# Optimization experiments

Measured on AMD Instinct MI355X. Metric: run time of the kernel, lower is better.

The kernel has to match this reference:

```python
import jax, jax.numpy as jnp
import numpy as np

N_NODES = 50000
N_EDGES = 800000
FEAT = 128
HIDDEN = 128
N_GRAPHS = 128


def setup_inputs() -> dict:
    key = jax.random.key(0)
    ks = jax.random.split(key, 12)
    x = jax.random.normal(ks[0], (N_NODES, FEAT), dtype=jnp.float32)
    # edges with no self loops (original add_remaining_self_loops drops existing
    # self loops and re-adds all of them; generating loop-free edges keeps the
    # reference simple and exactly equivalent)
    row = jax.random.randint(ks[1], (N_EDGES,), 0, N_NODES)
    off = jax.random.randint(ks[2], (N_EDGES,), 1, N_NODES)
    col = (row + off) % N_NODES
    edge_index = jnp.stack([row, col]).astype(jnp.int64)
    batch = jnp.sort(jax.random.randint(ks[3], (N_NODES,), 0, N_GRAPHS)).astype(jnp.int64)
    def glorot(k, fan_in, fan_out):
        s = np.sqrt(6.0 / (fan_in + fan_out))
        return jax.random.uniform(k, (fan_in, fan_out), jnp.float32, -s, s)
    W0 = glorot(ks[4], FEAT, HIDDEN)
    W1 = glorot(ks[5], HIDDEN, HIDDEN)
    W2 = glorot(ks[6], HIDDEN, HIDDEN)
    b0 = jnp.zeros((HIDDEN,), jnp.float32)
    b1 = jnp.zeros((HIDDEN,), jnp.float32)
    b2 = jnp.zeros((HIDDEN,), jnp.float32)
    return {"x": x, "edge_index": edge_index, "batch": batch,
            "W0": W0, "b0": b0, "W1": W1, "b1": b1, "W2": W2, "b2": b2}


def _gcn_norm(edge_index, num_nodes):
    # add self loops, compute symmetric normalization coeffs per edge
    loops = jnp.arange(num_nodes, dtype=edge_index.dtype)
    row = jnp.concatenate([edge_index[0], loops])
    col = jnp.concatenate([edge_index[1], loops])
    w = jnp.ones(row.shape[0], jnp.float32)
    deg = jax.ops.segment_sum(w, col, num_segments=num_nodes)
    dis = jnp.where(deg > 0, jax.lax.rsqrt(jnp.maximum(deg, 1e-30)), 0.0)
    norm = dis[row] * dis[col]
    return row, col, norm


def _gcn_layer(x, row, col, norm, W, b, num_nodes):
    h = x @ W                               # [N, H]
    msg = norm[:, None] * h[row]            # gather + scale  [E+N, H]
    out = jax.ops.segment_sum(msg, col, num_segments=num_nodes) + b
    return jax.nn.relu(out)


def reference(x, edge_index, batch, W0, b0, W1, b1, W2, b2):
    n = x.shape[0]
    row, col, norm = _gcn_norm(edge_index, n)
    x1 = _gcn_layer(x, row, col, norm, W0, b0, n)
    x2 = _gcn_layer(x1, row, col, norm, W1, b1, n)
    x3 = _gcn_layer(x2, row, col, norm, W2, b2, n)
    pools = [jax.ops.segment_sum(xi, batch, num_segments=N_GRAPHS)
             for xi in (x1, x2, x3)]
    global_rep = jnp.concatenate(pools, axis=1)  # [G, 3*H]
    return (global_rep, x3)
```

## Files before the change

### kernel.cpp

```cpp
#include <hip/hip_runtime.h>
#include <hip/hip_fp16.h>

#define N_NODES 50000
#define N_EDGES 800000
#define F 128
#define NG 128
#define POOL_W (3*F)
#define SCAN_CHUNK 1024
#define SCAN_BLKS ((N_NODES + SCAN_CHUNK - 1) / SCAN_CHUNK)

typedef _Float16 f16x8 __attribute__((ext_vector_type(8)));
typedef float f32x2 __attribute__((ext_vector_type(2)));
typedef float f32x4 __attribute__((ext_vector_type(4)));

__device__ __forceinline__ unsigned short f2h16(float f) {
    return __half_as_ushort(__float2half_rn(f));
}
__device__ __forceinline__ unsigned pkh2(float a, float b) {
    auto v = __builtin_amdgcn_cvt_pkrtz(a, b);
    union { decltype(v) h; unsigned u; } t;
    t.h = v;
    return t.u;
}
__device__ __forceinline__ void fma8(float* acc, uint2 v, float n) {
    f32x2 d;
    d = __builtin_amdgcn_cvt_pk_f32_fp8((int)v.x, false);
    acc[0] = fmaf(n, d[0], acc[0]); acc[1] = fmaf(n, d[1], acc[1]);
    d = __builtin_amdgcn_cvt_pk_f32_fp8((int)v.x, true);
    acc[2] = fmaf(n, d[0], acc[2]); acc[3] = fmaf(n, d[1], acc[3]);
    d = __builtin_amdgcn_cvt_pk_f32_fp8((int)v.y, false);
    acc[4] = fmaf(n, d[0], acc[4]); acc[5] = fmaf(n, d[1], acc[5]);
    d = __builtin_amdgcn_cvt_pk_f32_fp8((int)v.y, true);
    acc[6] = fmaf(n, d[0], acc[6]); acc[7] = fmaf(n, d[1], acc[7]);
}
__device__ __forceinline__ unsigned char f2fp8(float f) {
    return (unsigned char)(__builtin_amdgcn_cvt_pk_fp8_f32(f, f, 0, false) & 0xFF);
}
__device__ __forceinline__ float nrm_of(unsigned u) {
    return __half2float(__ushort_as_half((unsigned short)(u & 0xFFFFu)));
}

__global__ void k_init(int* __restrict__ cnt, float* __restrict__ pool,
                       const float* __restrict__ W0, const float* __restrict__ W1,
                       const float* __restrict__ W2, unsigned short* __restrict__ WT) {
    int i = blockIdx.x * 256 + threadIdx.x;
    if (i < N_NODES) cnt[i] = 0;
    if (i < NG * POOL_W) {
        pool[i] = 0.0f;
        int w = i >> 14, r = i & 16383;
        int k = r >> 7, c = r & 127;
        const float* W = (w == 0) ? W0 : (w == 1) ? W1 : W2;
        WT[(size_t)w * F * F + c * F + k] = f2h16(W[r]);
    }
}

__global__ void k_hist(const int* __restrict__ col, int* __restrict__ cnt,
                       unsigned short* __restrict__ seq) {
    int e2 = (blockIdx.x * 256 + threadIdx.x) * 2;
    if (e2 >= N_EDGES) return;
    int2 cc = *(const int2*)&col[e2];
    unsigned short s0 = (unsigned short)atomicAdd(&cnt[cc.x], 1);
    unsigned short s1 = (unsigned short)atomicAdd(&cnt[cc.y], 1);
    *(ushort2*)&seq[e2] = make_ushort2(s0, s1);
}

__global__ __launch_bounds__(256) void k_scan_red(const int* __restrict__ cnt,
                                                  int* __restrict__ part) {
    __shared__ int wsum[4];
    int i4 = blockIdx.x * SCAN_CHUNK + threadIdx.x * 4;
    int s;
    if (i4 + 3 < N_NODES) {
        int4 v = *(const int4*)&cnt[i4];
        s = v.x + v.y + v.z + v.w;
    } else {
        s = 0;
        #pragma unroll
        for (int j = 0; j < 4; ++j) if (i4 + j < N_NODES) s += cnt[i4 + j];
    }
    #pragma unroll
    for (int o = 32; o > 0; o >>= 1) s += __shfl_xor(s, o, 64);
    int lane = threadIdx.x & 63, w = threadIdx.x >> 6;
    if (lane == 0) wsum[w] = s;
    __syncthreads();
    if (threadIdx.x == 0) part[blockIdx.x] = wsum[0] + wsum[1] + wsum[2] + wsum[3];
}

__global__ __launch_bounds__(256) void k_scan_fin(const int* __restrict__ cnt,
                                                  const int* __restrict__ part,
                                                  int* __restrict__ rowptr,
                                                  float* __restrict__ dis) {
    __shared__ int wsum[4];
    __shared__ int sBase;
    int lane = threadIdx.x & 63, w = threadIdx.x >> 6;

    if (w == 0) {
        int v = (lane < SCAN_BLKS) ? part[lane] : 0;
        int s = v;
        #pragma unroll
        for (int o = 1; o < 64; o <<= 1) {
            int t = __shfl_up(s, o, 64);
            if (lane >= o) s += t;
        }
        if (lane == (int)blockIdx.x) sBase = s - v;
    }

    int i4 = blockIdx.x * SCAN_CHUNK + threadIdx.x * 4;
    int v[4];
    #pragma unroll
    for (int j = 0; j < 4; ++j) v[j] = (i4 + j < N_NODES) ? cnt[i4 + j] : 0;
    int ts = v[0] + v[1] + v[2] + v[3];
    int incl = ts;
    #pragma unroll
    for (int o = 1; o < 64; o <<= 1) {
        int t = __shfl_up(incl, o, 64);
        if (lane >= o) incl += t;
    }
    if (lane == 63) wsum[w] = incl;
    __syncthreads();
    if (threadIdx.x == 0) {
        int a = 0;
        #pragma unroll
        for (int t = 0; t < 4; ++t) { int b = wsum[t]; wsum[t] = a; a += b; }
    }
    __syncthreads();
    int base = sBase + wsum[w] + (incl - ts);
    int pre = 0;
    #pragma unroll
    for (int j = 0; j < 4; ++j) {
        int i = i4 + j;
        if (i <= N_NODES) rowptr[i] = base + pre;
        if (i < N_NODES) dis[i] = rsqrtf((float)v[j] + 1.0f);
        pre += v[j];
    }
}

__global__ void k_fill(const int* __restrict__ row, const int* __restrict__ col,
                       const unsigned short* __restrict__ seq,
                       const int* __restrict__ rowptr, const float* __restrict__ dis,
                       unsigned* __restrict__ csr) {
    int e2 = (blockIdx.x * 256 + threadIdx.x) * 2;
    if (e2 >= N_EDGES) return;
    int2 rr = *(const int2*)&row[e2];
    int2 cc = *(const int2*)&col[e2];
    ushort2 ss = *(const ushort2*)&seq[e2];
    int p0 = rowptr[cc.x] + (int)ss.x;
    csr[p0] = ((unsigned)rr.x << 16) | (unsigned)f2h16(dis[rr.x] * dis[cc.x]);
    int p1 = rowptr[cc.y] + (int)ss.y;
    csr[p1] = ((unsigned)rr.y << 16) | (unsigned)f2h16(dis[rr.y] * dis[cc.y]);
}

template <typename AIN>
__global__ __launch_bounds__(256) void k_gemm(const AIN* __restrict__ A,
                                              const unsigned short* __restrict__ WT,
                                              unsigned char* __restrict__ H) {
    __shared__ unsigned short sWT[F * 136];
    for (int t = threadIdx.x; t < F * 16; t += 256) {
        int c = t >> 4, ch = t & 15;
        *(uint4*)&sWT[c * 136 + ch * 8] = *(const uint4*)&WT[(size_t)c * F + ch * 8];
    }
    __syncthreads();

    int wave = threadIdx.x >> 6, lane = threadIdx.x & 63;
    int m = lane & 15, q = lane >> 4;
    int row = blockIdx.x * 64 + wave * 16 + m;
    int arow = (row < N_NODES) ? row : (N_NODES - 1);

    f32x4 acc[8];
    #pragma unroll
    for (int c = 0; c < 8; ++c) acc[c] = 0.f;

    #pragma unroll
    for (int kk = 0; kk < 4; ++kk) {
        int k0 = kk * 32 + q * 8;
        f16x8 a;
        if constexpr (sizeof(AIN) == 4) {
            const float* ap = &A[(size_t)arow * F + k0];
            float4 a0 = *(const float4*)ap;
            float4 a1 = *(const float4*)(ap + 4);
            a[0] = (_Float16)a0.x; a[1] = (_Float16)a0.y;
            a[2] = (_Float16)a0.z; a[3] = (_Float16)a0.w;
            a[4] = (_Float16)a1.x; a[5] = (_Float16)a1.y;
            a[6] = (_Float16)a1.z; a[7] = (_Float16)a1.w;
        } else {
            a = *(const f16x8*)&A[(size_t)arow * F + k0];
        }
        #pragma unroll
        for (int c = 0; c < 8; ++c) {
            f16x8 b = *(const f16x8*)&sWT[(c * 16 + m) * 136 + k0];
            acc[c] = __builtin_amdgcn_mfma_f32_16x16x32_f16(a, b, acc[c], 0, 0, 0);
        }
    }

    int rbase = blockIdx.x * 64 + wave * 16 + q * 4;
    #pragma unroll
    for (int c = 0; c < 8; ++c) {
        #pragma unroll
        for (int r = 0; r < 4; ++r) {
            int rr = rbase + r;
            if (rr < N_NODES) H[(size_t)rr * F + c * 16 + m] = f2fp8(acc[c][r]);
        }
    }
}

template <typename OUT>
__global__ __launch_bounds__(256) void k_agg(const unsigned char* __restrict__ h,
                                             const float* __restrict__ dis,
                                             const int* __restrict__ rowptr,
                                             const unsigned* __restrict__ csr,
                                             const float* __restrict__ bias,
                                             const int* __restrict__ batch,
                                             OUT* __restrict__ xout,
                                             float* __restrict__ pool) {
    int wave = threadIdx.x >> 6;
    int lane = threadIdx.x & 63;
    int g = lane >> 4;
    int l = lane & 15;
    int node = blockIdx.x * 4 + wave;

    float acc[8] = {0.f, 0.f, 0.f, 0.f, 0.f, 0.f, 0.f, 0.f};

    int s = rowptr[node], e = rowptr[node + 1];
    for (int base = s; base < e; base += 64) {
        int cnt = min(64, e - base);
        unsigned myent = (base + lane < e) ? csr[base + lane] : 0u;
        int nj = (cnt + 3) >> 2;
        #pragma unroll 4
        for (int j = 0; j < nj; ++j) {
            int src = g + 4 * j;
            unsigned ent = (unsigned)__shfl((int)myent, src, 64);
            if (src >= cnt) ent = 0u;
            uint2 v = *(const uint2*)(h + (size_t)(ent >> 16) * F + l * 8);
            fma8(acc, v, nrm_of(ent));
        }
    }

    #pragma unroll
    for (int j = 0; j < 8; ++j) {
        acc[j] += __shfl_xor(acc[j], 16, 64);
        acc[j] += __shfl_xor(acc[j], 32, 64);
    }

    float df = dis[node];
    uint2 sv = *(const uint2*)(h + (size_t)node * F + l * 8);
    fma8(acc, sv, df * df);
    float4 ba = *(const float4*)&bias[l * 8];
    float4 bb = *(const float4*)&bias[l * 8 + 4];
    acc[0] = fmaxf(acc[0] + ba.x, 0.f);
    acc[1] = fmaxf(acc[1] + ba.y, 0.f);
    acc[2] = fmaxf(acc[2] + ba.z, 0.f);
    acc[3] = fmaxf(acc[3] + ba.w, 0.f);
    acc[4] = fmaxf(acc[4] + bb.x, 0.f);
    acc[5] = fmaxf(acc[5] + bb.y, 0.f);
    acc[6] = fmaxf(acc[6] + bb.z, 0.f);
    acc[7] = fmaxf(acc[7] + bb.w, 0.f);

    if (g == 0) {
        if constexpr (sizeof(OUT) == 2) {
            uint4 o;
            o.x = pkh2(acc[0], acc[1]);
            o.y = pkh2(acc[2], acc[3]);
            o.z = pkh2(acc[4], acc[5]);
            o.w = pkh2(acc[6], acc[7]);
            *(uint4*)&xout[(size_t)node * F + l * 8] = o;
        } else {
            *(float4*)&xout[(size_t)node * F + l * 8] =
                make_float4(acc[0], acc[1], acc[2], acc[3]);
            *(float4*)&xout[(size_t)node * F + l * 8 + 4] =
                make_float4(acc[4], acc[5], acc[6], acc[7]);
        }
    }

    __shared__ float red[4][F];
    __shared__ int gsh[4];
    if (lane == 0) gsh[wave] = batch[node];
    if (g == 0) {
        *(float4*)&red[wave][l * 8]     = make_float4(acc[0], acc[1], acc[2], acc[3]);
        *(float4*)&red[wave][l * 8 + 4] = make_float4(acc[4], acc[5], acc[6], acc[7]);
    }
    __syncthreads();
    int g0 = gsh[0];
    bool uni = (gsh[1] == g0) & (gsh[2] == g0) & (gsh[3] == g0);
    if (uni) {
        if (threadIdx.x < F) {
            float ssum = red[0][threadIdx.x] + red[1][threadIdx.x]
                       + red[2][threadIdx.x] + red[3][threadIdx.x];
            atomicAdd(&pool[(size_t)g0 * POOL_W + threadIdx.x], ssum);
        }
    } else if (g == 0) {
        int gg = gsh[wave];
        #pragma unroll
        for (int j = 0; j < 8; ++j)
            atomicAdd(&pool[(size_t)gg * POOL_W + l * 8 + j], acc[j]);
    }
}

extern "C" void kernel_launch(void* const* d_in, const int* in_sizes, int n_in,
                              void* d_out, int out_size, void* d_ws, size_t ws_size,
                              hipStream_t stream) {
    const float* x    = (const float*)d_in[0];
    const int*   erow = (const int*)d_in[1];
    const int*   ecol = erow + N_EDGES;
    const int*   batch= (const int*)d_in[2];
    const float* W0   = (const float*)d_in[3];
    const float* b0   = (const float*)d_in[4];
    const float* W1   = (const float*)d_in[5];
    const float* b1   = (const float*)d_in[6];
    const float* W2   = (const float*)d_in[7];
    const float* b2   = (const float*)d_in[8];

    float* pool = (float*)d_out;
    float* x3   = (float*)d_out + NG * POOL_W;

    char* p = (char*)d_ws;
    auto carve = [&](size_t bytes) { char* q = p; p += (bytes + 255) & ~(size_t)255; return q; };
    float*          dis    = (float*)carve(N_NODES * 4);
    int*            cnt    = (int*)  carve(N_NODES * 4);
    int*            rowptr = (int*)  carve((N_NODES + 1) * 4);
    unsigned short* seq    = (unsigned short*)carve((size_t)N_EDGES * 2);
    int*            part   = (int*)  carve(SCAN_BLKS * 4);
    unsigned*       csr    = (unsigned*)carve((size_t)N_EDGES * 4);
    unsigned short* WT     = (unsigned short*)carve((size_t)3 * F * F * 2);
    unsigned char*  h      = (unsigned char*)carve((size_t)N_NODES * F);
    unsigned short* B      = (unsigned short*)carve((size_t)N_NODES * F * 2);

    const int nodeBlk  = (N_NODES + 255) / 256;
    const int edge2Blk = (N_EDGES / 2 + 255) / 256;
    const int aggBlk   = N_NODES / 4;
    const int gemmBlk  = (N_NODES + 63) / 64;

    k_init<<<nodeBlk, 256, 0, stream>>>(cnt, pool, W0, W1, W2, WT);
    k_hist<<<edge2Blk, 256, 0, stream>>>(ecol, cnt, seq);
    k_scan_red<<<SCAN_BLKS, 256, 0, stream>>>(cnt, part);
    k_scan_fin<<<SCAN_BLKS, 256, 0, stream>>>(cnt, part, rowptr, dis);
    k_fill<<<edge2Blk, 256, 0, stream>>>(erow, ecol, seq, rowptr, dis, csr);

    k_gemm<float><<<gemmBlk, 256, 0, stream>>>(x, WT + 0 * F * F, h);
    k_agg<unsigned short><<<aggBlk, 256, 0, stream>>>(h, dis, rowptr, csr, b0, batch, B, pool + 0 * F);

    k_gemm<unsigned short><<<gemmBlk, 256, 0, stream>>>(B, WT + 1 * F * F, h);
    k_agg<unsigned short><<<aggBlk, 256, 0, stream>>>(h, dis, rowptr, csr, b1, batch, B, pool + 1 * F);

    k_gemm<unsigned short><<<gemmBlk, 256, 0, stream>>>(B, WT + 2 * F * F, h);
    k_agg<float><<<aggBlk, 256, 0, stream>>>(h, dis, rowptr, csr, b2, batch, x3, pool + 2 * F);
}
```

Baseline: 216.6 us.

## Split feature dimension into two halves for cache-resident gather aggregation

Measured after the change: 254.8 us. +17.7%, slower.

```diff
diff --git a/kernel.cpp b/kernel.cpp
--- a/kernel.cpp
+++ b/kernel.cpp
@@ -22,16 +22,12 @@
     t.h = v;
     return t.u;
 }
-__device__ __forceinline__ void fma8(float* acc, uint2 v, float n) {
+__device__ __forceinline__ void fma4(float* acc, unsigned v, float n) {
     f32x2 d;
-    d = __builtin_amdgcn_cvt_pk_f32_fp8((int)v.x, false);
+    d = __builtin_amdgcn_cvt_pk_f32_fp8((int)v, false);
     acc[0] = fmaf(n, d[0], acc[0]); acc[1] = fmaf(n, d[1], acc[1]);
-    d = __builtin_amdgcn_cvt_pk_f32_fp8((int)v.x, true);
+    d = __builtin_amdgcn_cvt_pk_f32_fp8((int)v, true);
     acc[2] = fmaf(n, d[0], acc[2]); acc[3] = fmaf(n, d[1], acc[3]);
-    d = __builtin_amdgcn_cvt_pk_f32_fp8((int)v.y, false);
-    acc[4] = fmaf(n, d[0], acc[4]); acc[5] = fmaf(n, d[1], acc[5]);
-    d = __builtin_amdgcn_cvt_pk_f32_fp8((int)v.y, true);
-    acc[6] = fmaf(n, d[0], acc[6]); acc[7] = fmaf(n, d[1], acc[7]);
 }
 __device__ __forceinline__ unsigned char f2fp8(float f) {
     return (unsigned char)(__builtin_amdgcn_cvt_pk_fp8_f32(f, f, 0, false) & 0xFF);
@@ -152,7 +148,8 @@
 template <typename AIN>
 __global__ __launch_bounds__(256) void k_gemm(const AIN* __restrict__ A,
                                               const unsigned short* __restrict__ WT,
-                                              unsigned char* __restrict__ H) {
+                                              unsigned char* __restrict__ H0,
+                                              unsigned char* __restrict__ H1) {
     __shared__ unsigned short sWT[F * 136];
     for (int t = threadIdx.x; t < F * 16; t += 256) {
         int c = t >> 4, ch = t & 15;
@@ -194,10 +191,12 @@
     int rbase = blockIdx.x * 64 + wave * 16 + q * 4;
     #pragma unroll
     for (int c = 0; c < 8; ++c) {
+        unsigned char* H = (c < 4) ? H0 : H1;
+        int col = (c & 3) * 16 + m;
         #pragma unroll
         for (int r = 0; r < 4; ++r) {
             int rr = rbase + r;
-            if (rr < N_NODES) H[(size_t)rr * F + c * 16 + m] = f2fp8(acc[c][r]);
+            if (rr < N_NODES) H[(size_t)rr * 64 + col] = f2fp8(acc[c][r]);
         }
     }
 }
@@ -210,87 +209,80 @@
                                              const float* __restrict__ bias,
                                              const int* __restrict__ batch,
                                              OUT* __restrict__ xout,
-                                             float* __restrict__ pool) {
+                                             float* __restrict__ pool,
+                                             int fh) {
     int wave = threadIdx.x >> 6;
     int lane = threadIdx.x & 63;
     int g = lane >> 4;
     int l = lane & 15;
     int node = blockIdx.x * 4 + wave;
 
-    float acc[8] = {0.f, 0.f, 0.f, 0.f, 0.f, 0.f, 0.f, 0.f};
+    float acc[4] = {0.f, 0.f, 0.f, 0.f};
 
     int s = rowptr[node], e = rowptr[node + 1];
-    for (int base = s; base < e; base += 64) {
-        int cnt = min(64, e - base);
-        unsigned myent = (base + lane < e) ? csr[base + lane] : 0u;
-        int nj = (cnt + 3) >> 2;
-        #pragma unroll 4
-        for (int j = 0; j < nj; ++j) {
-            int src = g + 4 * j;
-            unsigned ent = (unsigned)__shfl((int)myent, src, 64);
-            if (src >= cnt) ent = 0u;
-            uint2 v = *(const uint2*)(h + (size_t)(ent >> 16) * F + l * 8);
-            fma8(acc, v, nrm_of(ent));
-        }
-    }
-
-    #pragma unroll
-    for (int j = 0; j < 8; ++j) {
+    int i = s + g;
+    unsigned c0 = (i      < e) ? csr[i]      : 0u;
+    unsigned c1 = (i + 4  < e) ? csr[i + 4]  : 0u;
+    unsigned c2 = (i + 8  < e) ? csr[i + 8]  : 0u;
+    unsigned c3 = (i + 12 < e) ? csr[i + 12] : 0u;
+    while (i < e) {
+        unsigned v0 = *(const unsigned*)(h + (size_t)(c0 >> 16) * 64 + l * 4);
+        unsigned v1 = *(const unsigned*)(h + (size_t)(c1 >> 16) * 64 + l * 4);
+        unsigned v2 = *(const unsigned*)(h + (size_t)(c2 >> 16) * 64 + l * 4);
+        unsigned v3 = *(const unsigned*)(h + (size_t)(c3 >> 16) * 64 + l * 4);
+        float n0 = nrm_of(c0), n1 = nrm_of(c1), n2 = nrm_of(c2), n3 = nrm_of(c3);
+        c0 = (i + 16 < e) ? csr[i + 16] : 0u;
+        c1 = (i + 20 < e) ? csr[i + 20] : 0u;
+        c2 = (i + 24 < e) ? csr[i + 24] : 0u;
+        c3 = (i + 28 < e) ? csr[i + 28] : 0u;
+        fma4(acc, v0, n0); fma4(acc, v1, n1); fma4(acc, v2, n2); fma4(acc, v3, n3);
+        i += 16;
+    }
+
+    #pragma unroll
+    for (int j = 0; j < 4; ++j) {
         acc[j] += __shfl_xor(acc[j], 16, 64);
         acc[j] += __shfl_xor(acc[j], 32, 64);
     }
 
     float df = dis[node];
-    uint2 sv = *(const uint2*)(h + (size_t)node * F + l * 8);
-    fma8(acc, sv, df * df);
-    float4 ba = *(const float4*)&bias[l * 8];
-    float4 bb = *(const float4*)&bias[l * 8 + 4];
+    unsigned sv = *(const unsigned*)(h + (size_t)node * 64 + l * 4);
+    fma4(acc, sv, df * df);
+    float4 ba = *(const float4*)&bias[fh * 64 + l * 4];
     acc[0] = fmaxf(acc[0] + ba.x, 0.f);
     acc[1] = fmaxf(acc[1] + ba.y, 0.f);
     acc[2] = fmaxf(acc[2] + ba.z, 0.f);
     acc[3] = fmaxf(acc[3] + ba.w, 0.f);
-    acc[4] = fmaxf(acc[4] + bb.x, 0.f);
-    acc[5] = fmaxf(acc[5] + bb.y, 0.f);
-    acc[6] = fmaxf(acc[6] + bb.z, 0.f);
-    acc[7] = fmaxf(acc[7] + bb.w, 0.f);
 
     if (g == 0) {
         if constexpr (sizeof(OUT) == 2) {
-            uint4 o;
-            o.x = pkh2(acc[0], acc[1]);
-            o.y = pkh2(acc[2], acc[3]);
-            o.z = pkh2(acc[4], acc[5]);
-            o.w = pkh2(acc[6], acc[7]);
-            *(uint4*)&xout[(size_t)node * F + l * 8] = o;
+            uint2 o = make_uint2(pkh2(acc[0], acc[1]), pkh2(acc[2], acc[3]));
+            *(uint2*)&xout[(size_t)node * F + fh * 64 + l * 4] = o;
         } else {
-            *(float4*)&xout[(size_t)node * F + l * 8] =
+            *(float4*)&xout[(size_t)node * F + fh * 64 + l * 4] =
                 make_float4(acc[0], acc[1], acc[2], acc[3]);
-            *(float4*)&xout[(size_t)node * F + l * 8 + 4] =
-                make_float4(acc[4], acc[5], acc[6], acc[7]);
-        }
-    }
-
-    __shared__ float red[4][F];
+        }
+    }
+
+    __shared__ float red[4][64];
     __shared__ int gsh[4];
     if (lane == 0) gsh[wave] = batch[node];
-    if (g == 0) {
-        *(float4*)&red[wave][l * 8]     = make_float4(acc[0], acc[1], acc[2], acc[3]);
-        *(float4*)&red[wave][l * 8 + 4] = make_float4(acc[4], acc[5], acc[6], acc[7]);
-    }
+    if (g == 0)
+        *(float4*)&red[wave][l * 4] = make_float4(acc[0], acc[1], acc[2], acc[3]);
     __syncthreads();
     int g0 = gsh[0];
     bool uni = (gsh[1] == g0) & (gsh[2] == g0) & (gsh[3] == g0);
     if (uni) {
-        if (threadIdx.x < F) {
+        if (threadIdx.x < 64) {
             float ssum = red[0][threadIdx.x] + red[1][threadIdx.x]
                        + red[2][threadIdx.x] + red[3][threadIdx.x];
-            atomicAdd(&pool[(size_t)g0 * POOL_W + threadIdx.x], ssum);
+            atomicAdd(&pool[(size_t)g0 * POOL_W + fh * 64 + threadIdx.x], ssum);
         }
     } else if (g == 0) {
         int gg = gsh[wave];
         #pragma unroll
-        for (int j = 0; j < 8; ++j)
-            atomicAdd(&pool[(size_t)gg * POOL_W + l * 8 + j], acc[j]);
+        for (int j = 0; j < 4; ++j)
+            atomicAdd(&pool[(size_t)gg * POOL_W + fh * 64 + l * 4 + j], acc[j]);
     }
 }
 
@@ -320,7 +312,8 @@
     int*            part   = (int*)  carve(SCAN_BLKS * 4);
     unsigned*       csr    = (unsigned*)carve((size_t)N_EDGES * 4);
     unsigned short* WT     = (unsigned short*)carve((size_t)3 * F * F * 2);
-    unsigned char*  h      = (unsigned char*)carve((size_t)N_NODES * F);
+    unsigned char*  h0     = (unsigned char*)carve((size_t)N_NODES * 64);
+    unsigned char*  h1     = (unsigned char*)carve((size_t)N_NODES * 64);
     unsigned short* B      = (unsigned short*)carve((size_t)N_NODES * F * 2);
 
     const int nodeBlk  = (N_NODES + 255) / 256;
@@ -334,12 +327,15 @@
     k_scan_fin<<<SCAN_BLKS, 256, 0, stream>>>(cnt, part, rowptr, dis);
     k_fill<<<edge2Blk, 256, 0, stream>>>(erow, ecol, seq, rowptr, dis, csr);
 
-    k_gemm<float><<<gemmBlk, 256, 0, stream>>>(x, WT + 0 * F * F, h);
-    k_agg<unsigned short><<<aggBlk, 256, 0, stream>>>(h, dis, rowptr, csr, b0, batch, B, pool + 0 * F);
-
-    k_gemm<unsigned short><<<gemmBlk, 256, 0, stream>>>(B, WT + 1 * F * F, h);
-    k_agg<unsigned short><<<aggBlk, 256, 0, stream>>>(h, dis, rowptr, csr, b1, batch, B, pool + 1 * F);
-
-    k_gemm<unsigned short><<<gemmBlk, 256, 0, stream>>>(B, WT + 2 * F * F, h);
-    k_agg<float><<<aggBlk, 256, 0, stream>>>(h, dis, rowptr, csr, b2, batch, x3, pool + 2 * F);
-}
+    k_gemm<float><<<gemmBlk, 256, 0, stream>>>(x, WT + 0 * F * F, h0, h1);
+    k_agg<unsigned short><<<aggBlk, 256, 0, stream>>>(h0, dis, rowptr, csr, b0, batch, B, pool + 0 * F, 0);
+    k_agg<unsigned short><<<aggBlk, 256, 0, stream>>>(h1, dis, rowptr, csr, b0, batch, B, pool + 0 * F, 1);
+
+    k_gemm<unsigned short><<<gemmBlk, 256, 0, stream>>>(B, WT + 1 * F * F, h0, h1);
+    k_agg<unsigned short><<<aggBlk, 256, 0, stream>>>(h0, dis, rowptr, csr, b1, batch, B, pool + 1 * F, 0);
+    k_agg<unsigned short><<<aggBlk, 256, 0, stream>>>(h1, dis, rowptr, csr, b1, batch, B, pool + 1 * F, 1);
+
+    k_gemm<unsigned short><<<gemmBlk, 256, 0, stream>>>(B, WT + 2 * F * F, h0, h1);
+    k_agg<float><<<aggBlk, 256, 0, stream>>>(h0, dis, rowptr, csr, b2, batch, x3, pool + 2 * F, 0);
+    k_agg<float><<<aggBlk, 256, 0, stream>>>(h1, dis, rowptr, csr, b2, batch, x3, pool + 2 * F, 1);
+}
```
